# Performance work log

Measured on AMD Instinct MI355X. Metric: run time of the kernel, lower is better.

Reference implementation:

```python
import jax, jax.numpy as jnp
import numpy as np

B, T, C, H, K = 16, 8192, 256, 256, 7


def setup_inputs() -> dict:
    key = jax.random.key(0)
    ks = jax.random.split(key, 6)
    x = jax.random.normal(ks[0], (B, T, C), dtype=jnp.float32)
    # ragged lengths in [T//2, T]; padding_mask: True = padding (at tail)
    lengths = jax.random.randint(ks[1], (B,), T // 2, T + 1)
    padding_mask = jnp.arange(T)[None, :] >= lengths[:, None]
    w1 = jax.random.normal(ks[2], (H, C, K), dtype=jnp.float32) / np.sqrt(C * K)
    b1 = jnp.zeros((H,), jnp.float32)
    w2 = jax.random.normal(ks[3], (H, H, 3), dtype=jnp.float32) / np.sqrt(H * 3)
    b2 = jnp.zeros((H,), jnp.float32)
    w3 = jax.random.normal(ks[4], (2, H, 1), dtype=jnp.float32) / np.sqrt(H)
    b3 = jnp.zeros((2,), jnp.float32)
    return {"x": x, "padding_mask": padding_mask,
            "w1": w1, "b1": b1, "w2": w2, "b2": b2, "w3": w3, "b3": b3}


def _conv1d(h, w, b, pad):
    # h: (B, Cin, T), w: (Cout, Cin, K) torch OIW layout
    y = jax.lax.conv_general_dilated(h, w, (1,), [(pad, pad)],
                                     dimension_numbers=("NCH", "OIH", "NCH"))
    return y + b[None, :, None]


def _boundary_logits(x, w1, b1, w2, b2, w3, b3):
    # RebornSegmenter.forward (dropout is identity in eval)
    h = jnp.transpose(x, (0, 2, 1))            # (B, C, T)
    h = jax.nn.relu(_conv1d(h, w1, b1, K // 2))
    h = jax.nn.relu(_conv1d(h, w2, b2, 1))
    h = _conv1d(h, w3, b3, 0)                  # (B, 2, T)
    return jnp.transpose(h, (0, 2, 1))         # (B, T, 2)


def _segment_pool(xb, sid):
    # xb: (T, C), sid: (T,) in [0, T] (T == dropped/padding)
    sums = jax.ops.segment_sum(xb, sid, num_segments=T)
    cnt = jax.ops.segment_sum(jnp.ones((T,), xb.dtype), sid, num_segments=T)
    return sums, cnt


def reference(x, padding_mask, w1, b1, w2, b2, w3, b3):
    # pre_segment with deterministic=True (boundary = argmax of conv logits)
    boundary_logits = _boundary_logits(x, w1, b1, w2, b2, w3, b3)
    boundary = jnp.argmax(boundary_logits, axis=-1)            # (B, T)
    is_b = (boundary == 1) & (~padding_mask)
    # token t belongs to segment = number of boundaries in [0..t]
    seg_id = jnp.cumsum(is_b.astype(jnp.int32), axis=1)
    seg_id = jnp.where(padding_mask, T, seg_id)  # out-of-range -> dropped
    sums, cnt = jax.vmap(_segment_pool)(x, seg_id)             # (B,T,C),(B,T)
    # segment mean; empty segments -> 0 (output padded to T segments, jit-safe;
    # torch crops to max segment count, extra columns here are flagged padded)
    new_logits = jnp.where(cnt[..., None] > 0,
                           sums / jnp.maximum(cnt, 1.0)[..., None], 0.0)
    nb = jnp.sum(is_b, axis=1)
    n_valid = jnp.where(jnp.any(~padding_mask, axis=1), nb + 1, 0)
    new_pad = jnp.arange(T)[None, :] >= n_valid[:, None]       # (B, T)
    return new_logits, new_pad
```

## Files before the change

### kernel.cpp

```cpp
#include <hip/hip_runtime.h>
#include <cstdint>
#include <cstddef>

#define BSZ 16
#define T   8192
#define CDIM 256
#define HDIM 256
#define KW  7

constexpr int BT = BSZ * T;
constexpr float TAU = 2e-3f;
constexpr int RCAP = 8192;

typedef __attribute__((ext_vector_type(8))) short short8;
typedef _Float16 half8 __attribute__((ext_vector_type(8)));
typedef __attribute__((ext_vector_type(4))) float f32x4;

constexpr size_t B_W1T  = 0;
constexpr size_t B_W2T  = B_W1T + 1835008;
constexpr size_t B_V    = B_W2T + 786432;
constexpr size_t B_D    = B_V + 1024;
constexpr size_t B_ISB  = B_D + 524288;
constexpr size_t B_SID  = B_ISB + 524288;
constexpr size_t B_SST  = B_SID + 524288;
constexpr size_t B_SEN  = B_SST + 524288;
constexpr size_t B_NV   = B_SEN + 524288;
constexpr size_t B_UCT  = B_NV + 64;
constexpr size_t B_UL   = B_UCT + 16;
constexpr size_t B_ZERO = B_UL + 32768;
constexpr size_t B_W1B  = B_ZERO + 256;
constexpr size_t B_W2B  = B_W1B + 917504;
constexpr size_t B_H1F  = B_W2B + 393216;
constexpr size_t B_DSUM = B_H1F + 25165824;

__device__ __forceinline__ void gl_lds16(const void* g, void* l) {
    __builtin_amdgcn_global_load_lds(
        (const __attribute__((address_space(1))) unsigned int*)g,
        (__attribute__((address_space(3))) unsigned int*)l,
        16, 0, 0);
}

__device__ __forceinline__ unsigned short f16_rne(float f) {
    _Float16 h = (_Float16)f;
    return __builtin_bit_cast(unsigned short, h);
}

__global__ void repack_kernel(const float* __restrict__ w1, const float* __restrict__ w2,
                              const float* __restrict__ w3,
                              float* __restrict__ W1R, float* __restrict__ W2R,
                              float* __restrict__ v,
                              unsigned short* __restrict__ W1b, unsigned short* __restrict__ W2b)
{
    int idx = blockIdx.x * blockDim.x + threadIdx.x;
    int stride = gridDim.x * blockDim.x;
    for (int i = idx; i < HDIM * 1792; i += stride) {
        int h = i / 1792, kc = i % 1792, kw = kc >> 8, c = kc & 255;
        float wv = w1[(size_t)h * 1792 + c * 7 + kw];
        W1R[i] = wv;
        W1b[i] = f16_rne(wv);
    }
    for (int i = idx; i < HDIM * 768; i += stride) {
        int h = i / 768, kc = i % 768, kw = kc >> 8, c = kc & 255;
        float wv = w2[(size_t)h * 768 + c * 3 + kw];
        W2R[i] = wv;
        W2b[i] = f16_rne(wv);
    }
    if (idx < HDIM) v[idx] = w3[HDIM + idx] - w3[idx];
}

__global__ __launch_bounds__(256) void xcast_kernel(const float* __restrict__ x,
                                                    unsigned short* __restrict__ xhf)
{
    size_t i = ((size_t)blockIdx.x * 256 + threadIdx.x) * 8;
    float4 a = *(const float4*)(x + i);
    float4 b = *(const float4*)(x + i + 4);
    short8 o;
    o[0] = (short)f16_rne(a.x); o[1] = (short)f16_rne(a.y);
    o[2] = (short)f16_rne(a.z); o[3] = (short)f16_rne(a.w);
    o[4] = (short)f16_rne(b.x); o[5] = (short)f16_rne(b.y);
    o[6] = (short)f16_rne(b.z); o[7] = (short)f16_rne(b.w);
    *(short8*)(xhf + i) = o;
}

__device__ __forceinline__ void c1_stageA(const unsigned short* xb, const unsigned short* zerobuf,
                                          half8* Ab, int t0, int c0, int lane, int wid)
{
    #pragma unroll
    for (int part = 0; part < 5; ++part) {
        int row = part * 64 + lane;
        int t = t0 + row - 3;
        const unsigned short* src = (row < 262 && t >= 0 && t < T)
            ? xb + (size_t)t * 256 + c0 + wid * 8 : zerobuf;
        gl_lds16(src, &Ab[wid * 322 + part * 64]);
    }
}
__device__ __forceinline__ void c1_stageB(const unsigned short* Wb, half8* Bb,
                                          int h0, int c0, int lane, int wid)
{
    #pragma unroll
    for (int s = 0; s < 14; ++s) {
        int bs = wid * 14 + s;
        int slot = bs >> 1, half = bs & 1;
        int kw = slot >> 2, bq = slot & 3;
        const unsigned short* src = Wb + (size_t)(h0 + half * 64 + lane) * 1792
                                    + kw * 256 + c0 + bq * 8;
        gl_lds16(src, &Bb[slot * 130 + half * 64]);
    }
}

__global__ __launch_bounds__(256) void conv1_mfma(
    const unsigned short* __restrict__ xhf,
    const unsigned short* __restrict__ Wb,
    const float* __restrict__ b1,
    const unsigned short* __restrict__ zerobuf,
    unsigned short* __restrict__ h1)
{
    __shared__ half8 A8[2][4 * 322];
    __shared__ half8 B8[2][28 * 130];
    const int tid = threadIdx.x, lane = tid & 63, wid = tid >> 6;
    const int b  = blockIdx.x >> 5;
    const int t0 = (blockIdx.x & 31) << 8;
    const int h0 = blockIdx.y << 7;
    const int q = lane >> 4, l15 = lane & 15;
    const unsigned short* xb = xhf + (size_t)b * T * 256;

    f32x4 acc[4][8] = {};

    c1_stageA(xb, zerobuf, A8[0], t0, 0, lane, wid);
    c1_stageB(Wb, B8[0], h0, 0, lane, wid);

    for (int cc = 0; cc < 8; ++cc) {
        const int cur = cc & 1;
        __syncthreads();
        if (cc < 7) {
            const int c1 = (cc + 1) << 5;
            c1_stageA(xb, zerobuf, A8[cur ^ 1], t0, c1, lane, wid);
            c1_stageB(Wb, B8[cur ^ 1], h0, c1, lane, wid);
        }
        #pragma unroll
        for (int kw = 0; kw < 7; ++kw) {
            half8 ah[4], bh[8];
            const int rbase = wid * 64 + l15 + kw;
            #pragma unroll
            for (int i = 0; i < 4; ++i) ah[i] = A8[cur][q * 322 + rbase + i * 16];
            #pragma unroll
            for (int j = 0; j < 8; ++j) bh[j] = B8[cur][(kw * 4 + q) * 130 + j * 16 + l15];
            #pragma unroll
            for (int i = 0; i < 4; ++i)
                #pragma unroll
                for (int j = 0; j < 8; ++j)
                    acc[i][j] = __builtin_amdgcn_mfma_f32_16x16x32_f16(ah[i], bh[j], acc[i][j], 0, 0, 0);
        }
    }
    #pragma unroll
    for (int j = 0; j < 8; ++j) {
        int h = h0 + j * 16 + l15;
        float bb = b1[h];
        #pragma unroll
        for (int i = 0; i < 4; ++i) {
            int tb = t0 + wid * 64 + i * 16 + q * 4;
            #pragma unroll
            for (int r = 0; r < 4; ++r)
                h1[(size_t)(b * T + tb + r) * 256 + h] = f16_rne(fmaxf(acc[i][j][r] + bb, 0.f));
        }
    }
}

__device__ __forceinline__ void c2_stageA(const unsigned short* hb, const unsigned short* zerobuf,
                                          half8* Ab, int t0, int c0, int lane, int wid)
{
    #pragma unroll
    for (int part = 0; part < 5; ++part) {
        int row = part * 64 + lane;
        int t = t0 + row - 1;
        const unsigned short* src = (row < 258 && t >= 0 && t < T)
            ? hb + (size_t)t * 256 + c0 + wid * 8 : zerobuf;
        gl_lds16(src, &Ab[wid * 322 + part * 64]);
    }
}
__device__ __forceinline__ void c2_stageB(const unsigned short* Wb, half8* Bb,
                                          int h0, int c0, int lane, int wid)
{
    #pragma unroll
    for (int s = 0; s < 6; ++s) {
        int bs = wid * 6 + s;
        int slot = bs >> 1, half = bs & 1;
        int kw = slot >> 2, bq = slot & 3;
        const unsigned short* src = Wb + (size_t)(h0 + half * 64 + lane) * 768
                                    + kw * 256 + c0 + bq * 8;
        gl_lds16(src, &Bb[slot * 130 + half * 64]);
    }
}

__global__ __launch_bounds__(256) void conv2_mfma(
    const unsigned short* __restrict__ h1,
    const unsigned short* __restrict__ Wb,
    const float* __restrict__ b2, const float* __restrict__ v,
    const unsigned short* __restrict__ zerobuf,
    float* __restrict__ dlog)
{
    __shared__ half8 A8[2][4 * 322];
    __shared__ half8 B8[2][12 * 130];
    const int tid = threadIdx.x, lane = tid & 63, wid = tid >> 6;
    const int b  = blockIdx.x >> 5;
    const int t0 = (blockIdx.x & 31) << 8;
    const int h0 = blockIdx.y << 7;
    const int q = lane >> 4, l15 = lane & 15;
    const unsigned short* hb = h1 + (size_t)b * T * 256;

    f32x4 acc[4][8] = {};

    c2_stageA(hb, zerobuf, A8[0], t0, 0, lane, wid);
    c2_stageB(Wb, B8[0], h0, 0, lane, wid);

    for (int cc = 0; cc < 8; ++cc) {
        const int cur = cc & 1;
        __syncthreads();
        if (cc < 7) {
            const int c1 = (cc + 1) << 5;
            c2_stageA(hb, zerobuf, A8[cur ^ 1], t0, c1, lane, wid);
            c2_stageB(Wb, B8[cur ^ 1], h0, c1, lane, wid);
        }
        #pragma unroll
        for (int kw = 0; kw < 3; ++kw) {
            half8 ah[4], bh[8];
            const int rbase = wid * 64 + l15 + kw;
            #pragma unroll
            for (int i = 0; i < 4; ++i) ah[i] = A8[cur][q * 322 + rbase + i * 16];
            #pragma unroll
            for (int j = 0; j < 8; ++j) bh[j] = B8[cur][(kw * 4 + q) * 130 + j * 16 + l15];
            #pragma unroll
            for (int i = 0; i < 4; ++i)
                #pragma unroll
                for (int j = 0; j < 8; ++j)
                    acc[i][j] = __builtin_amdgcn_mfma_f32_16x16x32_f16(ah[i], bh[j], acc[i][j], 0, 0, 0);
        }
    }
    float vv[8], bb[8];
    #pragma unroll
    for (int j = 0; j < 8; ++j) {
        int h = h0 + j * 16 + l15;
        vv[j] = v[h]; bb[j] = b2[h];
    }
    #pragma unroll
    for (int i = 0; i < 4; ++i) {
        int tb = t0 + wid * 64 + i * 16 + q * 4;
        #pragma unroll
        for (int r = 0; r < 4; ++r) {
            float s = 0.f;
            #pragma unroll
            for (int j = 0; j < 8; ++j)
                s += fmaxf(acc[i][j][r] + bb[j], 0.f) * vv[j];
            #pragma unroll
            for (int m = 1; m < 16; m <<= 1)
                s += __shfl_xor(s, m, 64);
            if (l15 == 0) atomicAdd(&dlog[b * T + tb + r], s);
        }
    }
}

__global__ void boundary_kernel(const float* __restrict__ d, const int* __restrict__ padmask,
                                const float* __restrict__ b3,
                                int* __restrict__ isb, int* __restrict__ ucount,
                                int* __restrict__ ulist)
{
    int bt = blockIdx.x * 256 + threadIdx.x;
    if (bt >= BT) return;
    int pad = padmask[bt];
    float dd = d[bt] + (b3[1] - b3[0]);
    isb[bt] = (pad == 0 && dd > 0.f) ? 1 : 0;
    if (pad == 0 && fabsf(dd) < TAU) {
        int slot = atomicAdd(ucount, 1);
        if (slot < RCAP) ulist[slot] = bt;
    }
}

__global__ __launch_bounds__(256) void recheck_h1(
    const float* __restrict__ x, const float* __restrict__ W1R,
    const float* __restrict__ b1, const float* __restrict__ zerof,
    const int* __restrict__ ulist, const int* __restrict__ ucount,
    float* __restrict__ h1f)
{
    __shared__ float xs[9 * CDIM];
    int n = *ucount; if (n > RCAP) n = RCAP;
    const int tid = threadIdx.x, lane = tid & 63, wid = tid >> 6;
    const int g = tid >> 4, l = tid & 15;
    const int nit = 4 * n;
    for (int item = blockIdx.x; item < nit; item += gridDim.x) {
        const int li = item >> 2, hc = item & 3;
        const int bt = ulist[li];
        const int b = bt >> 13, t = bt & (T - 1);
        __syncthreads();
        for (int r = wid; r < 9; r += 4) {
            int tt = t + r - 4;
            const float* src = (tt >= 0 && tt < T)
                ? x + (size_t)(b * T + tt) * CDIM + lane * 4 : zerof;
            gl_lds16(src, &xs[r * CDIM]);
        }
        __syncthreads();
        #pragma unroll
        for (int s = 0; s < 4; ++s) {
            const int h = hc * 64 + s * 16 + g;
            const float* wr = &W1R[(size_t)h * 1792];
            double p0 = 0.0, p1 = 0.0, p2 = 0.0;
            #pragma unroll 7
            for (int it = 0; it < 28; ++it) {
                const int e = it * 64 + l * 4;
                float4 w4 = *(const float4*)&wr[e];
                double w0 = (double)w4.x, w1v = (double)w4.y,
                       w2v = (double)w4.z, w3v = (double)w4.w;
                const float* x0 = &xs[e];
                p0 += w0 * (double)x0[0] + w1v * (double)x0[1]
                    + w2v * (double)x0[2] + w3v * (double)x0[3];
                const float* x1 = &xs[256 + e];
                p1 += w0 * (double)x1[0] + w1v * (double)x1[1]
                    + w2v * (double)x1[2] + w3v * (double)x1[3];
                const float* x2 = &xs[512 + e];
                p2 += w0 * (double)x2[0] + w1v * (double)x2[1]
                    + w2v * (double)x2[2] + w3v * (double)x2[3];
            }
            #pragma unroll
            for (int m = 1; m < 16; m <<= 1) {
                p0 += __shfl_xor(p0, m);
                p1 += __shfl_xor(p1, m);
                p2 += __shfl_xor(p2, m);
            }
            if (l == 0) {
                double bb = (double)b1[h];
                double a0 = bb + p0, a1 = bb + p1, a2 = bb + p2;
                float* o = &h1f[(size_t)li * 768];
                o[0 * 256 + h] = (t - 1 >= 0 && a0 > 0.0) ? (float)a0 : 0.f;
                o[1 * 256 + h] = (a1 > 0.0) ? (float)a1 : 0.f;
                o[2 * 256 + h] = (t + 1 < T && a2 > 0.0) ? (float)a2 : 0.f;
            }
        }
    }
}

__global__ __launch_bounds__(256) void recheck_h2(
    const float* __restrict__ h1f, const float* __restrict__ W2R,
    const float* __restrict__ b2, const float* __restrict__ w3,
    const int* __restrict__ ulist, const int* __restrict__ ucount,
    double* __restrict__ dsum)
{
    __shared__ float hs[768];
    __shared__ double red[64];
    int n = *ucount; if (n > RCAP) n = RCAP;
    const int tid = threadIdx.x, lane = tid & 63, wid = tid >> 6;
    const int g = tid >> 4, l = tid & 15;
    const int nit = 4 * n;
    for (int item = blockIdx.x; item < nit; item += gridDim.x) {
        const int li = item >> 2, hc = item & 3;
        __syncthreads();
        if (wid < 3)
            gl_lds16(h1f + (size_t)li * 768 + wid * 256 + lane * 4, &hs[wid * 256]);
        __syncthreads();
        #pragma unroll
        for (int s = 0; s < 4; ++s) {
            const int h = hc * 64 + s * 16 + g;
            const float* wr = &W2R[(size_t)h * 768];
            double c0 = 0.0;
            #pragma unroll
            for (int it = 0; it < 12; ++it) {
                const int e = it * 64 + l * 4;
                float4 w4 = *(const float4*)&wr[e];
                const float* hv = &hs[e];
                c0 += (double)w4.x * (double)hv[0] + (double)w4.y * (double)hv[1]
                    + (double)w4.z * (double)hv[2] + (double)w4.w * (double)hv[3];
            }
            #pragma unroll
            for (int m = 1; m < 16; m <<= 1) c0 += __shfl_xor(c0, m);
            if (l == 0) {
                double acc2 = (double)b2[h] + c0;
                double h2v = acc2 > 0.0 ? acc2 : 0.0;
                double vd = (double)w3[HDIM + h] - (double)w3[h];
                red[s * 16 + g] = vd * h2v;
            }
        }
        __syncthreads();
        if (tid < 32) red[tid] += red[tid + 32];
        __syncthreads();
        if (tid < 16) red[tid] += red[tid + 16];
        __syncthreads();
        if (tid == 0) {
            double ssum = 0.0;
            #pragma unroll
            for (int i = 0; i < 16; ++i) ssum += red[i];
            atomicAdd(&dsum[li], ssum);
        }
    }
}

__global__ void recheck_final(const double* __restrict__ dsum, const float* __restrict__ b3,
                              const int* __restrict__ ulist, const int* __restrict__ ucount,
                              int* __restrict__ isb)
{
    int n = *ucount; if (n > RCAP) n = RCAP;
    int li = blockIdx.x * 256 + threadIdx.x;
    if (li >= n) return;
    double dd = dsum[li] + ((double)b3[1] - (double)b3[0]);
    isb[ulist[li]] = (dd > 0.0) ? 1 : 0;
}

__global__ __launch_bounds__(1024) void scan_kernel(
    const int* __restrict__ isb, const int* __restrict__ padmask,
    int* __restrict__ sid, int* __restrict__ nvalid)
{
    __shared__ int ssum[1024];
    const int b = blockIdx.x, tid = threadIdx.x;
    const int base = b * T;
    int vals[8]; int s = 0;
    #pragma unroll
    for (int i = 0; i < 8; ++i) { vals[i] = isb[base + tid * 8 + i]; s += vals[i]; }
    ssum[tid] = s;
    __syncthreads();
    for (int off = 1; off < 1024; off <<= 1) {
        int add = (tid >= off) ? ssum[tid - off] : 0;
        __syncthreads();
        ssum[tid] += add;
        __syncthreads();
    }
    int run = ssum[tid] - s;
    #pragma unroll
    for (int i = 0; i < 8; ++i) {
        int t = tid * 8 + i;
        run += vals[i];
        sid[base + t] = (padmask[base + t] != 0) ? T : run;
    }
    if (tid == 1023) {
        int nb = ssum[1023];
        nvalid[b] = (padmask[base] == 0) ? (nb + 1) : 0;
    }
}

__global__ void segbounds_kernel(const int* __restrict__ sid, const int* __restrict__ padmask,
                                 int* __restrict__ sst, int* __restrict__ sen)
{
    int bt = blockIdx.x * 256 + threadIdx.x;
    if (bt >= BT) return;
    if (padmask[bt] != 0) return;
    int t = bt & (T - 1);
    int b = bt >> 13;
    int s = sid[bt];
    if (t == 0) {
        if (s < T) sst[b * T + s] = 0;
    } else if (s != sid[bt - 1]) {
        if (s < T) sst[b * T + s] = t;
    }
    bool last = (t == T - 1) || (padmask[bt + 1] != 0);
    if (s < T && (last || sid[bt + 1] != s)) sen[b * T + s] = t + 1;
}

__global__ __launch_bounds__(256) void pool_kernel(
    const float* __restrict__ x, const int* __restrict__ sst,
    const int* __restrict__ sen, const int* __restrict__ nvalid,
    float* __restrict__ out)
{
    int slot = blockIdx.x * 4 + (threadIdx.x >> 6);
    int lane = threadIdx.x & 63;
    int b = slot >> 13;
    int s = slot & (T - 1);
    int nv = nvalid[b];
    float4 res = make_float4(0.f, 0.f, 0.f, 0.f);
    if (s < nv) {
        int st = sst[slot], en = sen[slot];
        if (st >= 0 && en > st) {
            float4 a = make_float4(0.f, 0.f, 0.f, 0.f);
            const float* xp = &x[(size_t)(b * T + st) * CDIM + lane * 4];
            for (int t = st; t < en; ++t) {
                float4 xv = *(const float4*)xp;
                a.x += xv.x; a.y += xv.y; a.z += xv.z; a.w += xv.w;
                xp += CDIM;
            }
            float inv = 1.f / (float)(en - st);
            res = make_float4(a.x * inv, a.y * inv, a.z * inv, a.w * inv);
        }
    }
    *(float4*)&out[(size_t)slot * CDIM + lane * 4] = res;
    if (lane == 0) out[(size_t)BT * CDIM + slot] = (s < nv) ? 0.f : 1.f;
}

extern "C" void kernel_launch(void* const* d_in, const int* in_sizes, int n_in,
                              void* d_out, int out_size, void* d_ws, size_t ws_size,
                              hipStream_t stream)
{
    const float* x  = (const float*)d_in[0];
    const int* padmask = (const int*)d_in[1];
    const float* w1 = (const float*)d_in[2];
    const float* b1 = (const float*)d_in[3];
    const float* w2 = (const float*)d_in[4];
    const float* b2 = (const float*)d_in[5];
    const float* w3 = (const float*)d_in[6];
    const float* b3 = (const float*)d_in[7];

    char* ws = (char*)d_ws;
    float* W1R = (float*)(ws + B_W1T);
    float* W2R = (float*)(ws + B_W2T);
    float* v   = (float*)(ws + B_V);
    float* dlog = (float*)(ws + B_D);
    int* isb = (int*)(ws + B_ISB);
    int* sid = (int*)(ws + B_SID);
    int* sst = (int*)(ws + B_SST);
    int* sen = (int*)(ws + B_SEN);
    int* nv  = (int*)(ws + B_NV);
    int* uct = (int*)(ws + B_UCT);
    int* ul  = (int*)(ws + B_UL);
    unsigned short* zerobuf = (unsigned short*)(ws + B_ZERO);
    unsigned short* W1b = (unsigned short*)(ws + B_W1B);
    unsigned short* W2b = (unsigned short*)(ws + B_W2B);
    float* h1f = (float*)(ws + B_H1F);
    double* dsum = (double*)(ws + B_DSUM);

    float* out = (float*)d_out;
    unsigned short* h1  = (unsigned short*)out;
    unsigned short* xhf = h1 + (size_t)BT * 256;

    hipMemsetAsync(dlog, 0, BT * sizeof(float), stream);
    hipMemsetAsync(sst, 0xFF, BT * sizeof(int), stream);
    hipMemsetAsync(sen, 0xFF, BT * sizeof(int), stream);
    hipMemsetAsync(uct, 0, sizeof(int), stream);
    hipMemsetAsync(zerobuf, 0, 256, stream);
    hipMemsetAsync(dsum, 0, RCAP * sizeof(double), stream);

    repack_kernel<<<1024, 256, 0, stream>>>(w1, w2, w3, W1R, W2R, v, W1b, W2b);
    xcast_kernel<<<BT * 256 / (8 * 256), 256, 0, stream>>>(x, xhf);
    conv1_mfma<<<dim3(BSZ * (T / 256), HDIM / 128), 256, 0, stream>>>(
        xhf, W1b, b1, zerobuf, h1);
    conv2_mfma<<<dim3(BSZ * (T / 256), HDIM / 128), 256, 0, stream>>>(
        h1, W2b, b2, v, zerobuf, dlog);
    boundary_kernel<<<BT / 256, 256, 0, stream>>>(dlog, padmask, b3, isb, uct, ul);
    recheck_h1<<<4096, 256, 0, stream>>>(x, W1R, b1, (const float*)zerobuf, ul, uct, h1f);
    recheck_h2<<<4096, 256, 0, stream>>>(h1f, W2R, b2, w3, ul, uct, dsum);
    recheck_final<<<RCAP / 256, 256, 0, stream>>>(dsum, b3, ul, uct, isb);
    scan_kernel<<<BSZ, 1024, 0, stream>>>(isb, padmask, sid, nv);
    segbounds_kernel<<<BT / 256, 256, 0, stream>>>(sid, padmask, sst, sen);
    pool_kernel<<<BT / 4, 256, 0, stream>>>(x, sst, sen, nv, out);
}
```

Baseline: 708.0 us.

## Pre-tile activations and fp16 weights so conv loads read contiguous chunks

```diff
diff --git a/kernel.cpp b/kernel.cpp
--- a/kernel.cpp
+++ b/kernel.cpp
@@ -45,97 +45,120 @@
     return __builtin_bit_cast(unsigned short, h);
 }
 
+
 __global__ void repack_kernel(const float* __restrict__ w1, const float* __restrict__ w2,
                               const float* __restrict__ w3,
                               float* __restrict__ W1R, float* __restrict__ W2R,
                               float* __restrict__ v,
-                              unsigned short* __restrict__ W1b, unsigned short* __restrict__ W2b)
+                              unsigned short* __restrict__ W1bL, unsigned short* __restrict__ W2bL)
 {
     int idx = blockIdx.x * blockDim.x + threadIdx.x;
     int stride = gridDim.x * blockDim.x;
     for (int i = idx; i < HDIM * 1792; i += stride) {
         int h = i / 1792, kc = i % 1792, kw = kc >> 8, c = kc & 255;
-        float wv = w1[(size_t)h * 1792 + c * 7 + kw];
-        W1R[i] = wv;
-        W1b[i] = f16_rne(wv);
+        W1R[i] = w1[(size_t)h * 1792 + c * 7 + kw];
     }
     for (int i = idx; i < HDIM * 768; i += stride) {
         int h = i / 768, kc = i % 768, kw = kc >> 8, c = kc & 255;
-        float wv = w2[(size_t)h * 768 + c * 3 + kw];
-        W2R[i] = wv;
-        W2b[i] = f16_rne(wv);
+        W2R[i] = w2[(size_t)h * 768 + c * 3 + kw];
+    }
+    for (int o = idx; o < 2 * 8 * 28 * 1024; o += stride) {
+        int e = o & 7, lane = (o >> 3) & 63, half = (o >> 9) & 1;
+        int su = o >> 10;
+        int slot = su % 28, rest = su / 28;
+        int cc = rest & 7, h0g = rest >> 3;
+        int kw = slot >> 2, bq = slot & 3;
+        int h = h0g * 128 + half * 64 + lane;
+        int c = cc * 32 + bq * 8 + e;
+        W1bL[o] = f16_rne(w1[(size_t)h * 1792 + c * 7 + kw]);
+    }
+    for (int o = idx; o < 2 * 8 * 12 * 1024; o += stride) {
+        int e = o & 7, lane = (o >> 3) & 63, half = (o >> 9) & 1;
+        int su = o >> 10;
+        int slot = su % 12, rest = su / 12;
+        int cc = rest & 7, h0g = rest >> 3;
+        int kw = slot >> 2, bq = slot & 3;
+        int h = h0g * 128 + half * 64 + lane;
+        int c = cc * 32 + bq * 8 + e;
+        W2bL[o] = f16_rne(w2[(size_t)h * 768 + c * 3 + kw]);
     }
     if (idx < HDIM) v[idx] = w3[HDIM + idx] - w3[idx];
 }
 
 __global__ __launch_bounds__(256) void xcast_kernel(const float* __restrict__ x,
-                                                    unsigned short* __restrict__ xhf)
-{
-    size_t i = ((size_t)blockIdx.x * 256 + threadIdx.x) * 8;
-    float4 a = *(const float4*)(x + i);
-    float4 b = *(const float4*)(x + i + 4);
+                                                    unsigned short* __restrict__ xt)
+{
+    int j = blockIdx.x * 256 + threadIdx.x;
+    int rin = j & 255, wid = (j >> 8) & 3, cc = (j >> 10) & 7, grp = (j >> 13) & 31, b = j >> 18;
+    int t = grp * 256 + rin;
+    int c0 = cc * 32 + wid * 8;
+    const float* src = x + ((size_t)(b * T + t)) * 256 + c0;
+    float4 a = *(const float4*)src;
+    float4 bb = *(const float4*)(src + 4);
     short8 o;
     o[0] = (short)f16_rne(a.x); o[1] = (short)f16_rne(a.y);
     o[2] = (short)f16_rne(a.z); o[3] = (short)f16_rne(a.w);
-    o[4] = (short)f16_rne(b.x); o[5] = (short)f16_rne(b.y);
-    o[6] = (short)f16_rne(b.z); o[7] = (short)f16_rne(b.w);
-    *(short8*)(xhf + i) = o;
-}
-
-__device__ __forceinline__ void c1_stageA(const unsigned short* xb, const unsigned short* zerobuf,
-                                          half8* Ab, int t0, int c0, int lane, int wid)
+    o[4] = (short)f16_rne(bb.x); o[5] = (short)f16_rne(bb.y);
+    o[6] = (short)f16_rne(bb.z); o[7] = (short)f16_rne(bb.w);
+    *(short8*)(xt + (size_t)j * 8) = o;
+}
+
+__device__ __forceinline__ void c1_stageA(const unsigned short* xt, const unsigned short* zerobuf,
+                                          half8* Ab, int b, int t0, int cc, int lane, int wid)
 {
     #pragma unroll
     for (int part = 0; part < 5; ++part) {
         int row = part * 64 + lane;
         int t = t0 + row - 3;
-        const unsigned short* src = (row < 262 && t >= 0 && t < T)
-            ? xb + (size_t)t * 256 + c0 + wid * 8 : zerobuf;
+        const unsigned short* src = zerobuf;
+        if (row < 262 && t >= 0 && t < T) {
+            int grp = t >> 8, rin = t & 255;
+            src = xt + ((size_t)((((b * 32 + grp) * 8 + cc) * 4 + wid) * 256 + rin)) * 8;
+        }
         gl_lds16(src, &Ab[wid * 322 + part * 64]);
     }
 }
-__device__ __forceinline__ void c1_stageB(const unsigned short* Wb, half8* Bb,
-                                          int h0, int c0, int lane, int wid)
+__device__ __forceinline__ void c1_stageB(const unsigned short* WbL, half8* Bb,
+                                          int h0g8, int cc, int lane, int wid)
 {
     #pragma unroll
     for (int s = 0; s < 14; ++s) {
         int bs = wid * 14 + s;
         int slot = bs >> 1, half = bs & 1;
-        int kw = slot >> 2, bq = slot & 3;
-        const unsigned short* src = Wb + (size_t)(h0 + half * 64 + lane) * 1792
-                                    + kw * 256 + c0 + bq * 8;
+        const unsigned short* src = WbL
+            + ((size_t)(((h0g8 + cc) * 28 + slot) * 2 + half)) * 512 + lane * 8;
         gl_lds16(src, &Bb[slot * 130 + half * 64]);
     }
 }
 
 __global__ __launch_bounds__(256) void conv1_mfma(
-    const unsigned short* __restrict__ xhf,
-    const unsigned short* __restrict__ Wb,
+    const unsigned short* __restrict__ xt,
+    const unsigned short* __restrict__ WbL,
     const float* __restrict__ b1,
     const unsigned short* __restrict__ zerobuf,
-    unsigned short* __restrict__ h1)
+    unsigned short* __restrict__ h1t)
 {
     __shared__ half8 A8[2][4 * 322];
     __shared__ half8 B8[2][28 * 130];
     const int tid = threadIdx.x, lane = tid & 63, wid = tid >> 6;
     const int b  = blockIdx.x >> 5;
-    const int t0 = (blockIdx.x & 31) << 8;
+    const int grp = blockIdx.x & 31;
+    const int t0 = grp << 8;
     const int h0 = blockIdx.y << 7;
+    const int h0g8 = blockIdx.y * 8;
     const int q = lane >> 4, l15 = lane & 15;
-    const unsigned short* xb = xhf + (size_t)b * T * 256;
 
     f32x4 acc[4][8] = {};
 
-    c1_stageA(xb, zerobuf, A8[0], t0, 0, lane, wid);
-    c1_stageB(Wb, B8[0], h0, 0, lane, wid);
+    c1_stageA(xt, zerobuf, A8[0], b, t0, 0, lane, wid);
+    c1_stageB(WbL, B8[0], h0g8, 0, lane, wid);
 
     for (int cc = 0; cc < 8; ++cc) {
         const int cur = cc & 1;
         __syncthreads();
         if (cc < 7) {
-            const int c1 = (cc + 1) << 5;
-            c1_stageA(xb, zerobuf, A8[cur ^ 1], t0, c1, lane, wid);
-            c1_stageB(Wb, B8[cur ^ 1], h0, c1, lane, wid);
+            c1_stageA(xt, zerobuf, A8[cur ^ 1], b, t0, cc + 1, lane, wid);
+            c1_stageB(WbL, B8[cur ^ 1], h0g8, cc + 1, lane, wid);
         }
         #pragma unroll
         for (int kw = 0; kw < 7; ++kw) {
@@ -156,45 +179,49 @@
     for (int j = 0; j < 8; ++j) {
         int h = h0 + j * 16 + l15;
         float bb = b1[h];
+        int hcc = h >> 5, hwid = (h >> 3) & 3, he = h & 7;
+        size_t hbase = ((size_t)(((b * 32 + grp) * 8 + hcc) * 4 + hwid)) * 2048 + he;
         #pragma unroll
         for (int i = 0; i < 4; ++i) {
-            int tb = t0 + wid * 64 + i * 16 + q * 4;
+            int rb = wid * 64 + i * 16 + q * 4;
             #pragma unroll
             for (int r = 0; r < 4; ++r)
-                h1[(size_t)(b * T + tb + r) * 256 + h] = f16_rne(fmaxf(acc[i][j][r] + bb, 0.f));
-        }
-    }
-}
-
-__device__ __forceinline__ void c2_stageA(const unsigned short* hb, const unsigned short* zerobuf,
-                                          half8* Ab, int t0, int c0, int lane, int wid)
+                h1t[hbase + (size_t)(rb + r) * 8] = f16_rne(fmaxf(acc[i][j][r] + bb, 0.f));
+        }
+    }
+}
+
+__device__ __forceinline__ void c2_stageA(const unsigned short* ht, const unsigned short* zerobuf,
+                                          half8* Ab, int b, int t0, int cc, int lane, int wid)
 {
     #pragma unroll
     for (int part = 0; part < 5; ++part) {
         int row = part * 64 + lane;
         int t = t0 + row - 1;
-        const unsigned short* src = (row < 258 && t >= 0 && t < T)
-            ? hb + (size_t)t * 256 + c0 + wid * 8 : zerobuf;
+        const unsigned short* src = zerobuf;
+        if (row < 258 && t >= 0 && t < T) {
+            int grp = t >> 8, rin = t & 255;
+            src = ht + ((size_t)((((b * 32 + grp) * 8 + cc) * 4 + wid) * 256 + rin)) * 8;
+        }
         gl_lds16(src, &Ab[wid * 322 + part * 64]);
     }
 }
-__device__ __forceinline__ void c2_stageB(const unsigned short* Wb, half8* Bb,
-                                          int h0, int c0, int lane, int wid)
+__device__ __forceinline__ void c2_stageB(const unsigned short* WbL, half8* Bb,
+                                          int h0g8, int cc, int lane, int wid)
 {
     #pragma unroll
     for (int s = 0; s < 6; ++s) {
         int bs = wid * 6 + s;
         int slot = bs >> 1, half = bs & 1;
-        int kw = slot >> 2, bq = slot & 3;
-        const unsigned short* src = Wb + (size_t)(h0 + half * 64 + lane) * 768
-                                    + kw * 256 + c0 + bq * 8;
+        const unsigned short* src = WbL
+            + ((size_t)(((h0g8 + cc) * 12 + slot) * 2 + half)) * 512 + lane * 8;
         gl_lds16(src, &Bb[slot * 130 + half * 64]);
     }
 }
 
 __global__ __launch_bounds__(256) void conv2_mfma(
-    const unsigned short* __restrict__ h1,
-    const unsigned short* __restrict__ Wb,
+    const unsigned short* __restrict__ h1t,
+    const unsigned short* __restrict__ WbL,
     const float* __restrict__ b2, const float* __restrict__ v,
     const unsigned short* __restrict__ zerobuf,
     float* __restrict__ dlog)
@@ -205,21 +232,20 @@
     const int b  = blockIdx.x >> 5;
     const int t0 = (blockIdx.x & 31) << 8;
     const int h0 = blockIdx.y << 7;
+    const int h0g8 = blockIdx.y * 8;
     const int q = lane >> 4, l15 = lane & 15;
-    const unsigned short* hb = h1 + (size_t)b * T * 256;
 
     f32x4 acc[4][8] = {};
 
-    c2_stageA(hb, zerobuf, A8[0], t0, 0, lane, wid);
-    c2_stageB(Wb, B8[0], h0, 0, lane, wid);
+    c2_stageA(h1t, zerobuf, A8[0], b, t0, 0, lane, wid);
+    c2_stageB(WbL, B8[0], h0g8, 0, lane, wid);
 
     for (int cc = 0; cc < 8; ++cc) {
         const int cur = cc & 1;
         __syncthreads();
         if (cc < 7) {
-            const int c1 = (cc + 1) << 5;
-            c2_stageA(hb, zerobuf, A8[cur ^ 1], t0, c1, lane, wid);
-            c2_stageB(Wb, B8[cur ^ 1], h0, c1, lane, wid);
+            c2_stageA(h1t, zerobuf, A8[cur ^ 1], b, t0, cc + 1, lane, wid);
+            c2_stageB(WbL, B8[cur ^ 1], h0g8, cc + 1, lane, wid);
         }
         #pragma unroll
         for (int kw = 0; kw < 3; ++kw) {
@@ -506,14 +532,14 @@
     int* uct = (int*)(ws + B_UCT);
     int* ul  = (int*)(ws + B_UL);
     unsigned short* zerobuf = (unsigned short*)(ws + B_ZERO);
-    unsigned short* W1b = (unsigned short*)(ws + B_W1B);
-    unsigned short* W2b = (unsigned short*)(ws + B_W2B);
+    unsigned short* W1bL = (unsigned short*)(ws + B_W1B);
+    unsigned short* W2bL = (unsigned short*)(ws + B_W2B);
     float* h1f = (float*)(ws + B_H1F);
     double* dsum = (double*)(ws + B_DSUM);
 
     float* out = (float*)d_out;
-    unsigned short* h1  = (unsigned short*)out;
-    unsigned short* xhf = h1 + (size_t)BT * 256;
+    unsigned short* h1t = (unsigned short*)out;
+    unsigned short* xt  = h1t + (size_t)BT * 256;
 
     hipMemsetAsync(dlog, 0, BT * sizeof(float), stream);
     hipMemsetAsync(sst, 0xFF, BT * sizeof(int), stream);
@@ -522,12 +548,12 @@
     hipMemsetAsync(zerobuf, 0, 256, stream);
     hipMemsetAsync(dsum, 0, RCAP * sizeof(double), stream);
 
-    repack_kernel<<<1024, 256, 0, stream>>>(w1, w2, w3, W1R, W2R, v, W1b, W2b);
-    xcast_kernel<<<BT * 256 / (8 * 256), 256, 0, stream>>>(x, xhf);
+    repack_kernel<<<1024, 256, 0, stream>>>(w1, w2, w3, W1R, W2R, v, W1bL, W2bL);
+    xcast_kernel<<<BT * 256 / (8 * 256), 256, 0, stream>>>(x, xt);
     conv1_mfma<<<dim3(BSZ * (T / 256), HDIM / 128), 256, 0, stream>>>(
-        xhf, W1b, b1, zerobuf, h1);
+        xt, W1bL, b1, zerobuf, h1t);
     conv2_mfma<<<dim3(BSZ * (T / 256), HDIM / 128), 256, 0, stream>>>(
-        h1, W2b, b2, v, zerobuf, dlog);
+        h1t, W2bL, b2, v, zerobuf, dlog);
     boundary_kernel<<<BT / 256, 256, 0, stream>>>(dlog, padmask, b3, isb, uct, ul);
     recheck_h1<<<4096, 256, 0, stream>>>(x, W1R, b1, (const float*)zerobuf, ul, uct, h1f);
     recheck_h2<<<4096, 256, 0, stream>>>(h1f, W2R, b2, w3, ul, uct, dsum);
```

Measured after the change: 649.3 us. -8.3%, faster.
